# Optimization experiments

Hardware: AMD Instinct MI355X
Metric: run time of the kernel (lower is better)

## Reference

```python
import jax, jax.numpy as jnp
import numpy as np

N, H, M, B = 512, 64, 1024, 256
ETA = 1.0
INIT_STD = 0.01

def setup_inputs() -> dict:
    key = jax.random.key(0)
    k1, k2, k3, k4 = jax.random.split(key, 4)
    # Binary +/-1 sequences and memory (as produced upstream in the repo)
    sequences = jnp.where(jax.random.uniform(k1, (B, N)) < 0.5, -1.0, 1.0).astype(jnp.float32)
    memory = jnp.where(jax.random.uniform(k2, (M, N)) < 0.5, -1.0, 1.0).astype(jnp.float32)
    A_logits = (INIT_STD * jax.random.normal(k3, (N, H, N))).astype(jnp.float32)
    B_logits = (INIT_STD * jax.random.normal(k4, (H, N))).astype(jnp.float32)
    return {"sequences": sequences, "memory": memory, "A_logits": A_logits, "B_logits": B_logits}

def reference(sequences, memory, A_logits, B_logits):
    # Vectorized version of DAM.train_batch's loss over positions n=1..N-1.
    n_dim = sequences.shape[1]
    # Causal mask: row for position n attends to indices i < n. Rows n=1..N-1.
    ns = jnp.arange(1, n_dim)[:, None, None]            # (N-1,1,1)
    idx = jnp.arange(n_dim)[None, None, :]              # (1,1,N)
    mask = idx < ns                                      # (N-1,1,N)
    neg_inf = jnp.asarray(-jnp.inf, A_logits.dtype)
    A = jax.nn.softmax(jnp.where(mask, A_logits[1:], neg_inf), axis=-1)  # (N-1,H,N), zeros outside mask
    Bn = jax.nn.softmax(B_logits, axis=-1)               # (H,N)
    phi_mu = jnp.einsum('hn,mn->mh', Bn, memory)         # (M,H) memory keys
    hat_phi = jnp.einsum('bi,nhi->bnh', sequences, A)    # (B,N-1,H) queries for every position at once
    score = ETA * jnp.einsum('bnh,mh->bnm', hat_phi, phi_mu)  # (B,N-1,M)
    pi = jax.nn.softmax(score, axis=-1)                  # retrieval distribution over memories
    plus = (memory[:, 1:] > 0).astype(pi.dtype)          # (M,N-1): memory bit at position n is +1
    prob = jnp.einsum('bnm,mn->bn', pi, plus)            # P(next bit = +1)
    prob = jnp.clip(prob, 1e-6, 1.0 - 1e-6)
    target = (sequences[:, 1:] > 0).astype(prob.dtype)
    bce = -(target * jnp.log(prob) + (1.0 - target) * jnp.log1p(-prob))
    # mean over batch per position, summed over positions, / (N-1) == global mean
    return jnp.mean(bce)
```

## Files before the change

### kernel.cpp

```cpp
#include <hip/hip_runtime.h>
#include <stdint.h>

#define NPOS 512
#define NH   64
#define NM   1024
#define NB   256
#define NM1  511

typedef __attribute__((ext_vector_type(8)))  short bf16x8;
typedef __attribute__((ext_vector_type(16))) float f32x16;
typedef __attribute__((ext_vector_type(4)))  float f32x4;
typedef __attribute__((ext_vector_type(4)))  int   i32x4;

#if __has_builtin(__builtin_amdgcn_exp2f)
#define EXP2F(x) __builtin_amdgcn_exp2f(x)
#else
#define EXP2F(x) __expf((x) * 0.69314718055994531f)
#endif

__device__ __forceinline__ unsigned short f2bf(float x) {
    unsigned u = __float_as_uint(x);
    u = (u + 0x7FFFu + ((u >> 16) & 1u)) >> 16;
    return (unsigned short)u;
}
__device__ __forceinline__ int pack2(unsigned short a, unsigned short b) {
    return (int)a | ((int)b << 16);
}

__global__ __launch_bounds__(256, 4)
void kA_prep(const float* __restrict__ seq, const float* __restrict__ Bl,
             const float* __restrict__ mem,
             unsigned short* __restrict__ seq_bf, float* __restrict__ BnT,
             float* __restrict__ plusT, float* __restrict__ out) {
    const int bid = blockIdx.x, t = threadIdx.x;
    if (bid < 128) {
        if (bid == 0 && t == 0) out[0] = 0.f;
        int idx = (bid * 256 + t) * 4;
        f32x4 v = *(const f32x4*)(seq + idx);
        int2 o;
        o.x = pack2(f2bf(v.x), f2bf(v.y));
        o.y = pack2(f2bf(v.z), f2bf(v.w));
        *(int2*)(seq_bf + idx) = o;
    } else if (bid < 144) {
        const int h = (bid - 128) * 4 + (t >> 6), l = t & 63;
        float v[8]; float mx = -1e30f;
#pragma unroll
        for (int j = 0; j < 8; j++) { v[j] = Bl[h * NPOS + l + 64 * j]; mx = fmaxf(mx, v[j]); }
#pragma unroll
        for (int o = 32; o; o >>= 1) mx = fmaxf(mx, __shfl_xor(mx, o));
        float s = 0.f;
#pragma unroll
        for (int j = 0; j < 8; j++) { v[j] = __expf(v[j] - mx); s += v[j]; }
#pragma unroll
        for (int o = 32; o; o >>= 1) s += __shfl_xor(s, o);
        float r = 1.0f / s;
#pragma unroll
        for (int j = 0; j < 8; j++) BnT[(l + 64 * j) * NH + h] = v[j] * r;
    } else {
        __shared__ float sT[64][65];
        const int bb = bid - 144;
        const int mt = bb >> 3, nt = bb & 7;
        const int rr = t >> 2, cc = t & 3;
        const float* src = mem + (size_t)(mt * 64 + rr) * NPOS + nt * 64 + cc * 16;
#pragma unroll
        for (int j = 0; j < 4; j++) {
            f32x4 v = *(const f32x4*)(src + j * 4);
            sT[rr][cc * 16 + j * 4 + 0] = (v.x > 0.f) ? 1.f : 0.f;
            sT[rr][cc * 16 + j * 4 + 1] = (v.y > 0.f) ? 1.f : 0.f;
            sT[rr][cc * 16 + j * 4 + 2] = (v.z > 0.f) ? 1.f : 0.f;
            sT[rr][cc * 16 + j * 4 + 3] = (v.w > 0.f) ? 1.f : 0.f;
        }
        __syncthreads();
        float* dst = plusT + (size_t)(nt * 64 + rr) * NM + mt * 64 + cc * 16;
#pragma unroll
        for (int j = 0; j < 4; j++) {
            f32x4 o;
            o.x = sT[cc * 16 + j * 4 + 0][rr];
            o.y = sT[cc * 16 + j * 4 + 1][rr];
            o.z = sT[cc * 16 + j * 4 + 2][rr];
            o.w = sT[cc * 16 + j * 4 + 3][rr];
            *(f32x4*)(dst + j * 4) = o;
        }
    }
}

__global__ __launch_bounds__(256, 4)
void k1b_phimu(const float* __restrict__ BnT, const float* __restrict__ mem,
               unsigned short* __restrict__ phimu) {
    const int m0 = blockIdx.x * 2, t = threadIdx.x;
    __shared__ float mrow[2][NPOS];
    __shared__ float part[2][256];
    {
        int row = t >> 7, c = (t & 127) * 4;
        *(f32x4*)(&mrow[row][c]) = *(const f32x4*)(mem + (size_t)(m0 + row) * NPOS + c);
    }
    __syncthreads();
    const int h = t & 63, seg = t >> 6;
    float a[2] = {0.f, 0.f};
    float b2[2] = {0.f, 0.f};
    const float* bp = BnT + seg * 128 * NH + h;
#pragma unroll 8
    for (int nn = 0; nn < 128; nn += 2) {
        float x0 = bp[nn * NH], x1 = bp[(nn + 1) * NH];
#pragma unroll
        for (int row = 0; row < 2; row++) {
            a[row]  = fmaf(x0, mrow[row][seg * 128 + nn], a[row]);
            b2[row] = fmaf(x1, mrow[row][seg * 128 + nn + 1], b2[row]);
        }
    }
#pragma unroll
    for (int row = 0; row < 2; row++) part[row][t] = a[row] + b2[row];
    __syncthreads();
    if (t < 64) {
#pragma unroll
        for (int row = 0; row < 2; row++) {
            float s = (part[row][t] + part[row][t + 64]) + (part[row][t + 128] + part[row][t + 192]);
            phimu[(m0 + row) * NH + t] = f2bf(s * 1.4426950408889634f);
        }
    }
}

__global__ __launch_bounds__(256, 2)
void k23_fused(const float* __restrict__ Al, const unsigned short* __restrict__ seq_bf,
               const unsigned short* __restrict__ phimu, const float* __restrict__ plusT,
               const float* __restrict__ seq, float* __restrict__ out) {
    __shared__ __align__(16) unsigned short s_lds[256 * 72];
    __shared__ __align__(16) unsigned short e_lds[64 * 72];
    __shared__ float z_lds[64];
    __shared__ float s_plus[NM];

    const int t = threadIdx.x;
    const int n = NM1 - (int)blockIdx.x;
    const int ksteps = (n + 63) >> 6;
    const int wv = t >> 6, lane = t & 63, half = lane >> 5, r = lane & 31;

    if (t < 64) z_lds[t] = 0.f;
    *(f32x4*)(s_plus + t * 4) = *(const f32x4*)(plusT + n * NM + t * 4);

    const int eh = t >> 2, ei = (t & 3) * 16;
    const float* arow = Al + ((size_t)n * NH + eh) * NPOS + ei;
    const unsigned short* srcS = seq_bf + (size_t)t * NPOS;

    f32x16 acc00, acc01, acc10, acc11;
#pragma unroll
    for (int i = 0; i < 16; i++) { acc00[i] = 0.f; acc01[i] = 0.f; acc10[i] = 0.f; acc11[i] = 0.f; }

    f32x4 ea[4]; i32x4 sa[8];
#pragma unroll
    for (int g = 0; g < 4; g++) ea[g] = *(const f32x4*)(arow + g * 4);
#pragma unroll
    for (int c = 0; c < 8; c++) sa[c] = *(const i32x4*)(srcS + c * 8);
    __syncthreads();

    for (int kk = 0; kk < ksteps; kk++) {
        const int k0 = kk * 64;
        {
            float zp = 0.f;
            unsigned short* ep = e_lds + eh * 72 + ei;
#pragma unroll
            for (int g = 0; g < 4; g++) {
                int i0 = k0 + ei + g * 4;
                float e0 = (i0 + 0 < n) ? __expf(ea[g].x) : 0.f;
                float e1 = (i0 + 1 < n) ? __expf(ea[g].y) : 0.f;
                float e2 = (i0 + 2 < n) ? __expf(ea[g].z) : 0.f;
                float e3 = (i0 + 3 < n) ? __expf(ea[g].w) : 0.f;
                zp += (e0 + e1) + (e2 + e3);
                int2 o; o.x = pack2(f2bf(e0), f2bf(e1)); o.y = pack2(f2bf(e2), f2bf(e3));
                *(int2*)(ep + g * 4) = o;
            }
            zp += __shfl_xor(zp, 1);
            zp += __shfl_xor(zp, 2);
            if ((t & 3) == 0) z_lds[eh] += zp;
        }
        {
            unsigned short* dp = s_lds + t * 72;
#pragma unroll
            for (int c = 0; c < 8; c++) *(i32x4*)(dp + c * 8) = sa[c];
        }
        __syncthreads();
        if (kk + 1 < ksteps) {
#pragma unroll
            for (int g = 0; g < 4; g++) ea[g] = *(const f32x4*)(arow + k0 + 64 + g * 4);
#pragma unroll
            for (int c = 0; c < 8; c++) sa[c] = *(const i32x4*)(srcS + k0 + 64 + c * 8);
        }
        {
            const unsigned short* sA0 = s_lds + (wv * 64 + r) * 72;
            const unsigned short* sA1 = sA0 + 32 * 72;
            const unsigned short* sB0 = e_lds + r * 72;
            const unsigned short* sB1 = sB0 + 32 * 72;
#pragma unroll
            for (int kq = 0; kq < 4; kq++) {
                const int ko = kq * 16 + half * 8;
                bf16x8 A0 = *(const bf16x8*)(sA0 + ko);
                bf16x8 A1 = *(const bf16x8*)(sA1 + ko);
                bf16x8 B0 = *(const bf16x8*)(sB0 + ko);
                bf16x8 B1 = *(const bf16x8*)(sB1 + ko);
                acc00 = __builtin_amdgcn_mfma_f32_32x32x16_bf16(A0, B0, acc00, 0, 0, 0);
                acc01 = __builtin_amdgcn_mfma_f32_32x32x16_bf16(A0, B1, acc01, 0, 0, 0);
                acc10 = __builtin_amdgcn_mfma_f32_32x32x16_bf16(A1, B0, acc10, 0, 0, 0);
                acc11 = __builtin_amdgcn_mfma_f32_32x32x16_bf16(A1, B1, acc11, 0, 0, 0);
            }
        }
        __syncthreads();
    }
    {
        float rz0 = 1.0f / z_lds[r];
        float rz1 = 1.0f / z_lds[32 + r];
#pragma unroll
        for (int reg = 0; reg < 16; reg++) {
            int row = (reg & 3) + 8 * (reg >> 2) + 4 * half;
            s_lds[(wv * 64 + row) * 72 + r]            = f2bf(acc00[reg] * rz0);
            s_lds[(wv * 64 + row) * 72 + 32 + r]       = f2bf(acc01[reg] * rz1);
            s_lds[(wv * 64 + 32 + row) * 72 + r]       = f2bf(acc10[reg] * rz0);
            s_lds[(wv * 64 + 32 + row) * 72 + 32 + r]  = f2bf(acc11[reg] * rz1);
        }
    }
    __syncthreads();

    bf16x8 p[4];
#pragma unroll
    for (int kq = 0; kq < 4; kq++)
        p[kq] = *(const bf16x8*)(phimu + (r) * NH + kq * 16 + half * 8);
    bf16x8 q[2][4];
#pragma unroll
    for (int bs = 0; bs < 2; bs++)
#pragma unroll
        for (int kq = 0; kq < 4; kq++)
            q[bs][kq] = *(const bf16x8*)(s_lds + (wv * 64 + bs * 32 + r) * 72 + kq * 16 + half * 8);

    f32x4 den0 = {0.f,0.f,0.f,0.f}, num0 = {0.f,0.f,0.f,0.f};
    f32x4 den1 = {0.f,0.f,0.f,0.f}, num1 = {0.f,0.f,0.f,0.f};

    for (int it = 0; it < 32; ++it) {
        bf16x8 pn[4];
        if (it < 31) {
#pragma unroll
            for (int kq = 0; kq < 4; kq++)
                pn[kq] = *(const bf16x8*)(phimu + ((it + 1) * 32 + r) * NH + kq * 16 + half * 8);
        }
        f32x16 a0, a1;
#pragma unroll
        for (int i = 0; i < 16; i++) { a0[i] = 0.f; a1[i] = 0.f; }
#pragma unroll
        for (int kq = 0; kq < 4; kq++) {
            a0 = __builtin_amdgcn_mfma_f32_32x32x16_bf16(p[kq], q[0][kq], a0, 0, 0, 0);
            a1 = __builtin_amdgcn_mfma_f32_32x32x16_bf16(p[kq], q[1][kq], a1, 0, 0, 0);
        }
        const int mb = it * 32;
        f32x4 pv[4];
#pragma unroll
        for (int g = 0; g < 4; g++) pv[g] = *(const f32x4*)(s_plus + mb + 4 * half + 8 * g);
#pragma unroll
        for (int g = 0; g < 4; g++) {
            f32x4 e0, e1;
#pragma unroll
            for (int j = 0; j < 4; j++) {
                e0[j] = EXP2F(a0[4 * g + j]);
                e1[j] = EXP2F(a1[4 * g + j]);
            }
            den0 += e0; num0 += e0 * pv[g];
            den1 += e1; num1 += e1 * pv[g];
        }
        if (it < 31) {
#pragma unroll
            for (int kq = 0; kq < 4; kq++) p[kq] = pn[kq];
        }
    }
    float d0 = (den0[0] + den0[1]) + (den0[2] + den0[3]);
    float nu0 = (num0[0] + num0[1]) + (num0[2] + num0[3]);
    float d1 = (den1[0] + den1[1]) + (den1[2] + den1[3]);
    float nu1 = (num1[0] + num1[1]) + (num1[2] + num1[3]);
    d0 += __shfl_xor(d0, 32); nu0 += __shfl_xor(nu0, 32);
    d1 += __shfl_xor(d1, 32); nu1 += __shfl_xor(nu1, 32);

    float* dsum = (float*)e_lds;
    float* nsum = dsum + 256;
    if (half == 0) {
        dsum[wv * 64 + r]      = d0; nsum[wv * 64 + r]      = nu0;
        dsum[wv * 64 + 32 + r] = d1; nsum[wv * 64 + 32 + r] = nu1;
    }
    __syncthreads();
    {
        float dd = dsum[t], nn = nsum[t];
        float p2 = nn / dd;
        p2 = fminf(fmaxf(p2, 1e-6f), 1.0f - 1e-6f);
        float tg = seq[(size_t)t * NPOS + n];
        float bce = (tg > 0.f) ? -logf(p2) : -logf(1.0f - p2);
#pragma unroll
        for (int o = 32; o; o >>= 1) bce += __shfl_xor(bce, o);
        if (lane == 0) z_lds[wv] = bce;
    }
    __syncthreads();
    if (t == 0)
        atomicAdd(out, (z_lds[0] + z_lds[1] + z_lds[2] + z_lds[3]) * (1.0f / 130816.0f));
}

extern "C" void kernel_launch(void* const* d_in, const int* in_sizes, int n_in,
                              void* d_out, int out_size, void* d_ws, size_t ws_size,
                              hipStream_t stream) {
    const float* seq = (const float*)d_in[0];
    const float* mem = (const float*)d_in[1];
    const float* Al  = (const float*)d_in[2];
    const float* Bl  = (const float*)d_in[3];

    char* ws = (char*)d_ws;
    unsigned short* seq_bf = (unsigned short*)(ws + 0);
    float*          BnT    = (float*)(ws + 262144);
    unsigned short* phimu  = (unsigned short*)(ws + 393216);
    float*          plusT  = (float*)(ws + 524288);
    float*          outp   = (float*)d_out;

    kA_prep<<<272, 256, 0, stream>>>(seq, Bl, mem, seq_bf, BnT, plusT, outp);
    k1b_phimu<<<512, 256, 0, stream>>>(BnT, mem, phimu);
    k23_fused<<<511, 256, 0, stream>>>(Al, seq_bf, phimu, plusT, seq, outp);
}
```

Baseline: 145.2 us.

## Split fused attention-retrieval kernel across two batch halves per position

```diff
diff --git a/kernel.cpp b/kernel.cpp
--- a/kernel.cpp
+++ b/kernel.cpp
@@ -120,17 +120,18 @@
     }
 }
 
-__global__ __launch_bounds__(256, 2)
+__global__ __launch_bounds__(256, 4)
 void k23_fused(const float* __restrict__ Al, const unsigned short* __restrict__ seq_bf,
                const unsigned short* __restrict__ phimu, const float* __restrict__ plusT,
                const float* __restrict__ seq, float* __restrict__ out) {
-    __shared__ __align__(16) unsigned short s_lds[256 * 72];
+    __shared__ __align__(16) unsigned short s_lds[128 * 72];
     __shared__ __align__(16) unsigned short e_lds[64 * 72];
     __shared__ float z_lds[64];
     __shared__ float s_plus[NM];
 
     const int t = threadIdx.x;
-    const int n = NM1 - (int)blockIdx.x;
+    const int n = NM1 - (int)blockIdx.y;
+    const int bblk = (int)blockIdx.x;
     const int ksteps = (n + 63) >> 6;
     const int wv = t >> 6, lane = t & 63, half = lane >> 5, r = lane & 31;
 
@@ -139,17 +140,18 @@
 
     const int eh = t >> 2, ei = (t & 3) * 16;
     const float* arow = Al + ((size_t)n * NH + eh) * NPOS + ei;
-    const unsigned short* srcS = seq_bf + (size_t)t * NPOS;
-
-    f32x16 acc00, acc01, acc10, acc11;
-#pragma unroll
-    for (int i = 0; i < 16; i++) { acc00[i] = 0.f; acc01[i] = 0.f; acc10[i] = 0.f; acc11[i] = 0.f; }
-
-    f32x4 ea[4]; i32x4 sa[8];
+    const int srow = t >> 1, scol = (t & 1) * 32;
+    const unsigned short* srcS = seq_bf + (size_t)(bblk * 128 + srow) * NPOS + scol;
+
+    f32x16 acc0, acc1;
+#pragma unroll
+    for (int i = 0; i < 16; i++) { acc0[i] = 0.f; acc1[i] = 0.f; }
+
+    f32x4 ea[4]; i32x4 sa[4];
 #pragma unroll
     for (int g = 0; g < 4; g++) ea[g] = *(const f32x4*)(arow + g * 4);
 #pragma unroll
-    for (int c = 0; c < 8; c++) sa[c] = *(const i32x4*)(srcS + c * 8);
+    for (int c = 0; c < 4; c++) sa[c] = *(const i32x4*)(srcS + c * 8);
     __syncthreads();
 
     for (int kk = 0; kk < ksteps; kk++) {
@@ -173,33 +175,29 @@
             if ((t & 3) == 0) z_lds[eh] += zp;
         }
         {
-            unsigned short* dp = s_lds + t * 72;
-#pragma unroll
-            for (int c = 0; c < 8; c++) *(i32x4*)(dp + c * 8) = sa[c];
+            unsigned short* dp = s_lds + srow * 72 + scol;
+#pragma unroll
+            for (int c = 0; c < 4; c++) *(i32x4*)(dp + c * 8) = sa[c];
         }
         __syncthreads();
         if (kk + 1 < ksteps) {
 #pragma unroll
             for (int g = 0; g < 4; g++) ea[g] = *(const f32x4*)(arow + k0 + 64 + g * 4);
 #pragma unroll
-            for (int c = 0; c < 8; c++) sa[c] = *(const i32x4*)(srcS + k0 + 64 + c * 8);
+            for (int c = 0; c < 4; c++) sa[c] = *(const i32x4*)(srcS + k0 + 64 + c * 8);
         }
         {
-            const unsigned short* sA0 = s_lds + (wv * 64 + r) * 72;
-            const unsigned short* sA1 = sA0 + 32 * 72;
+            const unsigned short* sA  = s_lds + (wv * 32 + r) * 72;
             const unsigned short* sB0 = e_lds + r * 72;
             const unsigned short* sB1 = sB0 + 32 * 72;
 #pragma unroll
             for (int kq = 0; kq < 4; kq++) {
                 const int ko = kq * 16 + half * 8;
-                bf16x8 A0 = *(const bf16x8*)(sA0 + ko);
-                bf16x8 A1 = *(const bf16x8*)(sA1 + ko);
+                bf16x8 A  = *(const bf16x8*)(sA + ko);
                 bf16x8 B0 = *(const bf16x8*)(sB0 + ko);
                 bf16x8 B1 = *(const bf16x8*)(sB1 + ko);
-                acc00 = __builtin_amdgcn_mfma_f32_32x32x16_bf16(A0, B0, acc00, 0, 0, 0);
-                acc01 = __builtin_amdgcn_mfma_f32_32x32x16_bf16(A0, B1, acc01, 0, 0, 0);
-                acc10 = __builtin_amdgcn_mfma_f32_32x32x16_bf16(A1, B0, acc10, 0, 0, 0);
-                acc11 = __builtin_amdgcn_mfma_f32_32x32x16_bf16(A1, B1, acc11, 0, 0, 0);
+                acc0 = __builtin_amdgcn_mfma_f32_32x32x16_bf16(A, B0, acc0, 0, 0, 0);
+                acc1 = __builtin_amdgcn_mfma_f32_32x32x16_bf16(A, B1, acc1, 0, 0, 0);
             }
         }
         __syncthreads();
@@ -210,47 +208,48 @@
 #pragma unroll
         for (int reg = 0; reg < 16; reg++) {
             int row = (reg & 3) + 8 * (reg >> 2) + 4 * half;
-            s_lds[(wv * 64 + row) * 72 + r]            = f2bf(acc00[reg] * rz0);
-            s_lds[(wv * 64 + row) * 72 + 32 + r]       = f2bf(acc01[reg] * rz1);
-            s_lds[(wv * 64 + 32 + row) * 72 + r]       = f2bf(acc10[reg] * rz0);
-            s_lds[(wv * 64 + 32 + row) * 72 + 32 + r]  = f2bf(acc11[reg] * rz1);
-        }
-    }
-    __syncthreads();
-
-    bf16x8 p[4];
+            s_lds[(wv * 32 + row) * 72 + r]      = f2bf(acc0[reg] * rz0);
+            s_lds[(wv * 32 + row) * 72 + 32 + r] = f2bf(acc1[reg] * rz1);
+        }
+    }
+    __syncthreads();
+
+    bf16x8 p0[4], p1[4];
+#pragma unroll
+    for (int kq = 0; kq < 4; kq++) {
+        p0[kq] = *(const bf16x8*)(phimu + (r) * NH + kq * 16 + half * 8);
+        p1[kq] = *(const bf16x8*)(phimu + (32 + r) * NH + kq * 16 + half * 8);
+    }
+    bf16x8 q[4];
 #pragma unroll
     for (int kq = 0; kq < 4; kq++)
-        p[kq] = *(const bf16x8*)(phimu + (r) * NH + kq * 16 + half * 8);
-    bf16x8 q[2][4];
-#pragma unroll
-    for (int bs = 0; bs < 2; bs++)
-#pragma unroll
-        for (int kq = 0; kq < 4; kq++)
-            q[bs][kq] = *(const bf16x8*)(s_lds + (wv * 64 + bs * 32 + r) * 72 + kq * 16 + half * 8);
-
-    f32x4 den0 = {0.f,0.f,0.f,0.f}, num0 = {0.f,0.f,0.f,0.f};
-    f32x4 den1 = {0.f,0.f,0.f,0.f}, num1 = {0.f,0.f,0.f,0.f};
-
-    for (int it = 0; it < 32; ++it) {
-        bf16x8 pn[4];
-        if (it < 31) {
-#pragma unroll
-            for (int kq = 0; kq < 4; kq++)
-                pn[kq] = *(const bf16x8*)(phimu + ((it + 1) * 32 + r) * NH + kq * 16 + half * 8);
-        }
+        q[kq] = *(const bf16x8*)(s_lds + (wv * 32 + r) * 72 + kq * 16 + half * 8);
+
+    f32x4 den = {0.f,0.f,0.f,0.f}, num = {0.f,0.f,0.f,0.f};
+
+    for (int it = 0; it < 16; ++it) {
         f32x16 a0, a1;
 #pragma unroll
         for (int i = 0; i < 16; i++) { a0[i] = 0.f; a1[i] = 0.f; }
 #pragma unroll
         for (int kq = 0; kq < 4; kq++) {
-            a0 = __builtin_amdgcn_mfma_f32_32x32x16_bf16(p[kq], q[0][kq], a0, 0, 0, 0);
-            a1 = __builtin_amdgcn_mfma_f32_32x32x16_bf16(p[kq], q[1][kq], a1, 0, 0, 0);
-        }
-        const int mb = it * 32;
-        f32x4 pv[4];
-#pragma unroll
-        for (int g = 0; g < 4; g++) pv[g] = *(const f32x4*)(s_plus + mb + 4 * half + 8 * g);
+            a0 = __builtin_amdgcn_mfma_f32_32x32x16_bf16(p0[kq], q[kq], a0, 0, 0, 0);
+            a1 = __builtin_amdgcn_mfma_f32_32x32x16_bf16(p1[kq], q[kq], a1, 0, 0, 0);
+        }
+        if (it < 15) {
+#pragma unroll
+            for (int kq = 0; kq < 4; kq++) {
+                p0[kq] = *(const bf16x8*)(phimu + ((it * 2 + 2) * 32 + r) * NH + kq * 16 + half * 8);
+                p1[kq] = *(const bf16x8*)(phimu + ((it * 2 + 3) * 32 + r) * NH + kq * 16 + half * 8);
+            }
+        }
+        const int mb0 = it * 64, mb1 = it * 64 + 32;
+        f32x4 pv0[4], pv1[4];
+#pragma unroll
+        for (int g = 0; g < 4; g++) {
+            pv0[g] = *(const f32x4*)(s_plus + mb0 + 4 * half + 8 * g);
+            pv1[g] = *(const f32x4*)(s_plus + mb1 + 4 * half + 8 * g);
+        }
 #pragma unroll
         for (int g = 0; g < 4; g++) {
             f32x4 e0, e1;
@@ -259,38 +258,24 @@
                 e0[j] = EXP2F(a0[4 * g + j]);
                 e1[j] = EXP2F(a1[4 * g + j]);
             }
-            den0 += e0; num0 += e0 * pv[g];
-            den1 += e1; num1 += e1 * pv[g];
-        }
-        if (it < 31) {
-#pragma unroll
-            for (int kq = 0; kq < 4; kq++) p[kq] = pn[kq];
-        }
-    }
-    float d0 = (den0[0] + den0[1]) + (den0[2] + den0[3]);
-    float nu0 = (num0[0] + num0[1]) + (num0[2] + num0[3]);
-    float d1 = (den1[0] + den1[1]) + (den1[2] + den1[3]);
-    float nu1 = (num1[0] + num1[1]) + (num1[2] + num1[3]);
-    d0 += __shfl_xor(d0, 32); nu0 += __shfl_xor(nu0, 32);
-    d1 += __shfl_xor(d1, 32); nu1 += __shfl_xor(nu1, 32);
-
-    float* dsum = (float*)e_lds;
-    float* nsum = dsum + 256;
+            den += e0; num += e0 * pv0[g];
+            den += e1; num += e1 * pv1[g];
+        }
+    }
+    float d  = (den[0] + den[1]) + (den[2] + den[3]);
+    float nu = (num[0] + num[1]) + (num[2] + num[3]);
+    d += __shfl_xor(d, 32); nu += __shfl_xor(nu, 32);
+
+    float bce = 0.f;
     if (half == 0) {
-        dsum[wv * 64 + r]      = d0; nsum[wv * 64 + r]      = nu0;
-        dsum[wv * 64 + 32 + r] = d1; nsum[wv * 64 + 32 + r] = nu1;
-    }
-    __syncthreads();
-    {
-        float dd = dsum[t], nn = nsum[t];
-        float p2 = nn / dd;
+        float p2 = nu / d;
         p2 = fminf(fmaxf(p2, 1e-6f), 1.0f - 1e-6f);
-        float tg = seq[(size_t)t * NPOS + n];
-        float bce = (tg > 0.f) ? -logf(p2) : -logf(1.0f - p2);
-#pragma unroll
-        for (int o = 32; o; o >>= 1) bce += __shfl_xor(bce, o);
-        if (lane == 0) z_lds[wv] = bce;
-    }
+        float tg = seq[(size_t)(bblk * 128 + wv * 32 + r) * NPOS + n];
+        bce = (tg > 0.f) ? -logf(p2) : -logf(1.0f - p2);
+    }
+#pragma unroll
+    for (int o = 32; o; o >>= 1) bce += __shfl_xor(bce, o);
+    if (lane == 0) z_lds[wv] = bce;
     __syncthreads();
     if (t == 0)
         atomicAdd(out, (z_lds[0] + z_lds[1] + z_lds[2] + z_lds[3]) * (1.0f / 130816.0f));
@@ -313,5 +298,5 @@
 
     kA_prep<<<272, 256, 0, stream>>>(seq, Bl, mem, seq_bf, BnT, plusT, outp);
     k1b_phimu<<<512, 256, 0, stream>>>(BnT, mem, phimu);
-    k23_fused<<<511, 256, 0, stream>>>(Al, seq_bf, phimu, plusT, seq, outp);
-}
+    k23_fused<<<dim3(2, 511), 256, 0, stream>>>(Al, seq_bf, phimu, plusT, seq, outp);
+}
```

Measured after the change: 172.1 us. 1.19x slower.

## Load sequence MFMA operands from global directly and double-buffer exp tile

Applied to the files above, without the earlier changes.

```diff
diff --git a/kernel.cpp b/kernel.cpp
--- a/kernel.cpp
+++ b/kernel.cpp
@@ -124,10 +124,9 @@
 void k23_fused(const float* __restrict__ Al, const unsigned short* __restrict__ seq_bf,
                const unsigned short* __restrict__ phimu, const float* __restrict__ plusT,
                const float* __restrict__ seq, float* __restrict__ out) {
-    __shared__ __align__(16) unsigned short s_lds[256 * 72];
-    __shared__ __align__(16) unsigned short e_lds[64 * 72];
+    __shared__ __align__(16) unsigned short big[256 * 72];
+    __shared__ float s_plus[NM];
     __shared__ float z_lds[64];
-    __shared__ float s_plus[NM];
 
     const int t = threadIdx.x;
     const int n = NM1 - (int)blockIdx.x;
@@ -139,24 +138,23 @@
 
     const int eh = t >> 2, ei = (t & 3) * 16;
     const float* arow = Al + ((size_t)n * NH + eh) * NPOS + ei;
-    const unsigned short* srcS = seq_bf + (size_t)t * NPOS;
+    const unsigned short* s0 = seq_bf + (size_t)(wv * 64 + r) * NPOS + half * 8;
+    const unsigned short* s1 = s0 + 32 * NPOS;
 
     f32x16 acc00, acc01, acc10, acc11;
 #pragma unroll
     for (int i = 0; i < 16; i++) { acc00[i] = 0.f; acc01[i] = 0.f; acc10[i] = 0.f; acc11[i] = 0.f; }
 
-    f32x4 ea[4]; i32x4 sa[8];
+    f32x4 ea[4];
 #pragma unroll
     for (int g = 0; g < 4; g++) ea[g] = *(const f32x4*)(arow + g * 4);
-#pragma unroll
-    for (int c = 0; c < 8; c++) sa[c] = *(const i32x4*)(srcS + c * 8);
-    __syncthreads();
 
     for (int kk = 0; kk < ksteps; kk++) {
         const int k0 = kk * 64;
+        unsigned short* ebuf = big + (kk & 1) * (64 * 72);
         {
             float zp = 0.f;
-            unsigned short* ep = e_lds + eh * 72 + ei;
+            int ev[8];
 #pragma unroll
             for (int g = 0; g < 4; g++) {
                 int i0 = k0 + ei + g * 4;
@@ -165,55 +163,49 @@
                 float e2 = (i0 + 2 < n) ? __expf(ea[g].z) : 0.f;
                 float e3 = (i0 + 3 < n) ? __expf(ea[g].w) : 0.f;
                 zp += (e0 + e1) + (e2 + e3);
-                int2 o; o.x = pack2(f2bf(e0), f2bf(e1)); o.y = pack2(f2bf(e2), f2bf(e3));
-                *(int2*)(ep + g * 4) = o;
+                ev[g * 2]     = pack2(f2bf(e0), f2bf(e1));
+                ev[g * 2 + 1] = pack2(f2bf(e2), f2bf(e3));
             }
+            unsigned short* ep = ebuf + eh * 72 + ei;
+            *(i32x4*)(ep)     = *(i32x4*)(ev);
+            *(i32x4*)(ep + 8) = *(i32x4*)(ev + 4);
             zp += __shfl_xor(zp, 1);
             zp += __shfl_xor(zp, 2);
             if ((t & 3) == 0) z_lds[eh] += zp;
         }
+        if (kk + 1 < ksteps) {
+#pragma unroll
+            for (int g = 0; g < 4; g++) ea[g] = *(const f32x4*)(arow + k0 + 64 + g * 4);
+        }
+        __syncthreads();
         {
-            unsigned short* dp = s_lds + t * 72;
-#pragma unroll
-            for (int c = 0; c < 8; c++) *(i32x4*)(dp + c * 8) = sa[c];
-        }
-        __syncthreads();
-        if (kk + 1 < ksteps) {
-#pragma unroll
-            for (int g = 0; g < 4; g++) ea[g] = *(const f32x4*)(arow + k0 + 64 + g * 4);
-#pragma unroll
-            for (int c = 0; c < 8; c++) sa[c] = *(const i32x4*)(srcS + k0 + 64 + c * 8);
-        }
-        {
-            const unsigned short* sA0 = s_lds + (wv * 64 + r) * 72;
-            const unsigned short* sA1 = sA0 + 32 * 72;
-            const unsigned short* sB0 = e_lds + r * 72;
+            const unsigned short* sB0 = ebuf + r * 72;
             const unsigned short* sB1 = sB0 + 32 * 72;
 #pragma unroll
             for (int kq = 0; kq < 4; kq++) {
-                const int ko = kq * 16 + half * 8;
-                bf16x8 A0 = *(const bf16x8*)(sA0 + ko);
-                bf16x8 A1 = *(const bf16x8*)(sA1 + ko);
-                bf16x8 B0 = *(const bf16x8*)(sB0 + ko);
-                bf16x8 B1 = *(const bf16x8*)(sB1 + ko);
+                const int ko = kq * 16;
+                bf16x8 A0 = *(const bf16x8*)(s0 + k0 + ko);
+                bf16x8 A1 = *(const bf16x8*)(s1 + k0 + ko);
+                bf16x8 B0 = *(const bf16x8*)(sB0 + ko + half * 8);
+                bf16x8 B1 = *(const bf16x8*)(sB1 + ko + half * 8);
                 acc00 = __builtin_amdgcn_mfma_f32_32x32x16_bf16(A0, B0, acc00, 0, 0, 0);
                 acc01 = __builtin_amdgcn_mfma_f32_32x32x16_bf16(A0, B1, acc01, 0, 0, 0);
                 acc10 = __builtin_amdgcn_mfma_f32_32x32x16_bf16(A1, B0, acc10, 0, 0, 0);
                 acc11 = __builtin_amdgcn_mfma_f32_32x32x16_bf16(A1, B1, acc11, 0, 0, 0);
             }
         }
-        __syncthreads();
-    }
+    }
+    __syncthreads();
     {
         float rz0 = 1.0f / z_lds[r];
         float rz1 = 1.0f / z_lds[32 + r];
 #pragma unroll
         for (int reg = 0; reg < 16; reg++) {
             int row = (reg & 3) + 8 * (reg >> 2) + 4 * half;
-            s_lds[(wv * 64 + row) * 72 + r]            = f2bf(acc00[reg] * rz0);
-            s_lds[(wv * 64 + row) * 72 + 32 + r]       = f2bf(acc01[reg] * rz1);
-            s_lds[(wv * 64 + 32 + row) * 72 + r]       = f2bf(acc10[reg] * rz0);
-            s_lds[(wv * 64 + 32 + row) * 72 + 32 + r]  = f2bf(acc11[reg] * rz1);
+            big[(wv * 64 + row) * 72 + r]            = f2bf(acc00[reg] * rz0);
+            big[(wv * 64 + row) * 72 + 32 + r]       = f2bf(acc01[reg] * rz1);
+            big[(wv * 64 + 32 + row) * 72 + r]       = f2bf(acc10[reg] * rz0);
+            big[(wv * 64 + 32 + row) * 72 + 32 + r]  = f2bf(acc11[reg] * rz1);
         }
     }
     __syncthreads();
@@ -227,7 +219,7 @@
     for (int bs = 0; bs < 2; bs++)
 #pragma unroll
         for (int kq = 0; kq < 4; kq++)
-            q[bs][kq] = *(const bf16x8*)(s_lds + (wv * 64 + bs * 32 + r) * 72 + kq * 16 + half * 8);
+            q[bs][kq] = *(const bf16x8*)(big + (wv * 64 + bs * 32 + r) * 72 + kq * 16 + half * 8);
 
     f32x4 den0 = {0.f,0.f,0.f,0.f}, num0 = {0.f,0.f,0.f,0.f};
     f32x4 den1 = {0.f,0.f,0.f,0.f}, num1 = {0.f,0.f,0.f,0.f};
@@ -274,23 +266,20 @@
     d0 += __shfl_xor(d0, 32); nu0 += __shfl_xor(nu0, 32);
     d1 += __shfl_xor(d1, 32); nu1 += __shfl_xor(nu1, 32);
 
-    float* dsum = (float*)e_lds;
-    float* nsum = dsum + 256;
+    float bce = 0.f;
     if (half == 0) {
-        dsum[wv * 64 + r]      = d0; nsum[wv * 64 + r]      = nu0;
-        dsum[wv * 64 + 32 + r] = d1; nsum[wv * 64 + 32 + r] = nu1;
-    }
-    __syncthreads();
-    {
-        float dd = dsum[t], nn = nsum[t];
-        float p2 = nn / dd;
-        p2 = fminf(fmaxf(p2, 1e-6f), 1.0f - 1e-6f);
-        float tg = seq[(size_t)t * NPOS + n];
-        float bce = (tg > 0.f) ? -logf(p2) : -logf(1.0f - p2);
-#pragma unroll
-        for (int o = 32; o; o >>= 1) bce += __shfl_xor(bce, o);
-        if (lane == 0) z_lds[wv] = bce;
-    }
+        float pa = nu0 / d0;
+        pa = fminf(fmaxf(pa, 1e-6f), 1.0f - 1e-6f);
+        float ta = seq[(size_t)(wv * 64 + r) * NPOS + n];
+        bce += (ta > 0.f) ? -logf(pa) : -logf(1.0f - pa);
+        float pb = nu1 / d1;
+        pb = fminf(fmaxf(pb, 1e-6f), 1.0f - 1e-6f);
+        float tb = seq[(size_t)(wv * 64 + 32 + r) * NPOS + n];
+        bce += (tb > 0.f) ? -logf(pb) : -logf(1.0f - pb);
+    }
+#pragma unroll
+    for (int o = 32; o; o >>= 1) bce += __shfl_xor(bce, o);
+    if (lane == 0) z_lds[wv] = bce;
     __syncthreads();
     if (t == 0)
         atomicAdd(out, (z_lds[0] + z_lds[1] + z_lds[2] + z_lds[3]) * (1.0f / 130816.0f));
```

After: 147.1 us. About the same (+1.3%).
